# Kernel tuning notes

Hardware: AMD Instinct MI355X
Metric: run time of the kernel (lower is better)

The kernel has to match this reference:

```python
import math
import jax, jax.numpy as jnp
import numpy as np

B, L, D, H = 2, 1024, 1024, 16
HD = D // H
NBUCKETS = 64
EPS = 1e-5


def _rotary(x, pos):
    # x: (B,H,L,hd), pos: (B,L) float positions
    hd = x.shape[-1]
    nf = hd // 2
    periods = jnp.exp(jnp.linspace(math.log(1.0), math.log(10000.0), nf))
    freqs = 2.0 * np.pi / periods
    freqs = jnp.concatenate([freqs, freqs], axis=-1)  # (hd,)
    ang = pos[:, None, :, None].astype(x.dtype) * freqs  # (B,1,L,hd)
    cos, sin = jnp.cos(ang), jnp.sin(ang)
    x1, x2 = jnp.split(x, 2, axis=-1)
    rot = jnp.concatenate([-x2, x1], axis=-1)
    return x * cos + rot * sin


def _layernorm(x, g, b):
    mu = jnp.mean(x, axis=-1, keepdims=True)
    var = jnp.mean((x - mu) ** 2, axis=-1, keepdims=True)
    return (x - mu) * jax.lax.rsqrt(var + EPS) * g + b


def setup_inputs() -> dict:
    key = jax.random.key(0)
    ks = jax.random.split(key, 16)
    s = 1.0 / math.sqrt(D)
    x = jax.random.normal(ks[0], (B, L, D), jnp.float32)
    z = jax.random.randint(ks[1], (B, L, L), 0, NBUCKETS, jnp.int32)
    mask = jnp.ones((B, L), dtype=bool)
    idx = jnp.tile(jnp.arange(L, dtype=jnp.int32)[None, :], (B, 1))
    chain = jnp.sort(jax.random.randint(ks[2], (B, L), 0, 4, jnp.int32), axis=-1)
    mol_type = jax.random.randint(ks[3], (B, L), 0, 2, jnp.int32)
    Wq = jax.random.normal(ks[4], (D, D), jnp.float32) * s
    Wk = jax.random.normal(ks[5], (D, D), jnp.float32) * s
    Wv = jax.random.normal(ks[6], (D, D), jnp.float32) * s
    Wo = jax.random.normal(ks[7], (D, D), jnp.float32) * s
    cWq = jax.random.normal(ks[8], (D, D), jnp.float32) * s
    cWk = jax.random.normal(ks[9], (D, D), jnp.float32) * s
    cWv = jax.random.normal(ks[10], (D, D), jnp.float32) * s
    qg = jnp.ones((D,), jnp.float32)
    qb = jnp.zeros((D,), jnp.float32)
    kg = jnp.ones((D,), jnp.float32)
    kb = jnp.zeros((D,), jnp.float32)
    attn_bias = jax.random.normal(ks[11], (NBUCKETS, H), jnp.float32) * 0.02
    return dict(x=x, z=z, mask=mask, idx=idx, chain=chain, mol_type=mol_type,
                Wq=Wq, Wk=Wk, Wv=Wv, Wo=Wo, cWq=cWq, cWk=cWk, cWv=cWv,
                qg=qg, qb=qb, kg=kg, kb=kb, attn_bias=attn_bias)


def reference(x, z, mask, idx, chain, mol_type, Wq, Wk, Wv, Wo, cWq, cWk, cWv,
              qg, qb, kg, kb, attn_bias):
    scale = 1.0 / math.sqrt(HD)  # sqrt(D / heads)

    def split_heads(t):  # (B,L,D) -> (B,H,L,hd)
        return t.reshape(B, L, H, HD).transpose(0, 2, 1, 3)

    q = split_heads(_layernorm(x @ Wq.T, qg, qb))
    k = split_heads(_layernorm(x @ Wk.T, kg, kb))
    q = _rotary(q, idx)
    k = _rotary(k, idx)
    attn = jnp.einsum('bhqd,bhkd->bhqk', q, k) * scale

    cq = split_heads(x @ cWq.T)
    ck = split_heads(x @ cWk.T)
    cross_attn = jnp.einsum('bhqd,bhkd->bhqk', cq, ck) * scale

    # same polymer chain mask (B,L,L)
    spm = (chain[:, None, :] == chain[:, :, None]) & (mol_type == 0)[:, None, :]
    attn = jnp.where(spm[:, None], attn, cross_attn)

    # gathered pairwise bias: bias[z] (B,L,L,H) -> (B,H,L,L)
    attn = attn + attn_bias[z].transpose(0, 3, 1, 2)

    attn = jnp.where(mask[:, None, None, :], attn, -jnp.inf)
    attn = jax.nn.softmax(attn, axis=-1)

    self_w = jnp.where(spm[:, None], attn, 0.0)
    cross_w = jnp.where(spm[:, None], 0.0, attn)

    v = split_heads(x @ Wv.T)
    v = _rotary(v, idx)  # rope_values
    out = jnp.einsum('bhqk,bhkd->bhqd', self_w, v)
    out = _rotary(out, -idx)
    out = out.transpose(0, 2, 1, 3).reshape(B, L, D)

    cv = split_heads(x @ cWv.T)
    cross_out = jnp.einsum('bhqk,bhkd->bhqd', cross_w, cv)
    cross_out = cross_out.transpose(0, 2, 1, 3).reshape(B, L, D)

    return (out + cross_out) @ Wo.T
```

## Files before the change

### kernel.cpp

```cpp
#include <hip/hip_runtime.h>


typedef __attribute__((ext_vector_type(8))) short short8;
typedef __attribute__((ext_vector_type(4))) short short4v;
typedef __attribute__((ext_vector_type(4))) float f32x4;

struct W6 { const unsigned short* p[6]; };
struct Src13 { const void* p[13]; };

__device__ __forceinline__ float bf2f(unsigned short u){
  union { unsigned u32; float f; } v; v.u32 = ((unsigned)u) << 16; return v.f;
}
__device__ __forceinline__ unsigned short f2bf(float f){
  unsigned u = __float_as_uint(f);
  u += 0x7FFFu + ((u >> 16) & 1u);
  return (unsigned short)(u >> 16);
}
__device__ __forceinline__ unsigned short f2bf_rz(float f){
  return (unsigned short)(__float_as_uint(f) >> 16);
}
__device__ __forceinline__ void async16(const void* g, void* l){
  __builtin_amdgcn_global_load_lds(
      (const __attribute__((address_space(1))) unsigned int*)g,
      (__attribute__((address_space(3))) unsigned int*)l, 16, 0, 0);
}
__device__ __forceinline__ f32x4 mfma16(short8 a, short8 b, f32x4 c){
  return __builtin_amdgcn_mfma_f32_16x16x32_bf16(a, b, c, 0, 0, 0);
}
__device__ __forceinline__ float freq_of(int dd){
  return 6.283185307179586f * __expf(-0.29710775393471563f * (float)dd);
}

#define PX   0
#define PW(i) (2097152 + (i) * 1048576)
#define PQG  9437184
#define PQB  9438208
#define PKG  9439232
#define PKB  9440256
#define PBI  9441280
#define PARK_TOTAL 9442304

__global__ __launch_bounds__(256) void k_convert(
    Src13 src, unsigned short* __restrict__ park,
    const int* __restrict__ z, unsigned char* __restrict__ zpk,
    int* __restrict__ flag)
{
  const int t = threadIdx.x;
  const int bid = blockIdx.x;
  if (bid >= 9221) {
    int base = (bid - 9221) * 1024 + t * 4;
    int4 zv = *(const int4*)(z + base);
    unsigned int pk = (unsigned)zv.x | ((unsigned)zv.y << 8) |
                      ((unsigned)zv.z << 16) | ((unsigned)zv.w << 24);
    *(unsigned int*)(zpk + base) = pk;
    return;
  }
  __shared__ int shcnt;
  if (t == 0) shcnt = 0;
  __syncthreads();
  const unsigned short* xr = (const unsigned short*)src.p[0];
  int e = (xr[2 * t] >> 7) & 0xFF;
  unsigned long long m = __ballot(e >= 132);
  if ((t & 63) == 0) atomicAdd(&shcnt, __popcll(m));
  __syncthreads();
  const bool isf32 = shcnt > 64;

  int seg, inner;
  if (bid < 2048)      { seg = 0;                        inner = bid; }
  else if (bid < 9216) { seg = 1 + ((bid - 2048) >> 10); inner = (bid - 2048) & 1023; }
  else                 { seg = 8 + (bid - 9216);         inner = 0; }
  static const __device__ int segbase[13] = {
    PX, PW(0), PW(1), PW(2), PW(3), PW(4), PW(5), PW(6),
    PQG, PQB, PKG, PKB, PBI };
  unsigned short* dst = park + segbase[seg] + inner * 1024 + t * 4;
  if (isf32) {
    const float* s = (const float*)src.p[seg] + inner * 1024 + t * 4;
    f32x4 v = *(const f32x4*)s;
    short4v o;
    o.x = (short)f2bf(v.x); o.y = (short)f2bf(v.y);
    o.z = (short)f2bf(v.z); o.w = (short)f2bf(v.w);
    *(short4v*)dst = o;
  } else {
    const unsigned short* s = (const unsigned short*)src.p[seg] + inner * 1024 + t * 4;
    *(short4v*)dst = *(const short4v*)s;
  }
  if (bid == 0 && t == 0) *flag = isf32 ? 1 : 0;
}

__global__ __launch_bounds__(256, 2) void k_proj_gemm(
    const unsigned short* __restrict__ X, W6 w6, unsigned short* __restrict__ Y)
{
  __shared__ unsigned short As[2][128 * 32];
  __shared__ unsigned short Bs[2][128 * 32];
  const int t = threadIdx.x;
  const int lane = t & 63, wid = t >> 6;
  int bid = blockIdx.y * 16 + blockIdx.x;
  bid = (bid & 7) * 96 + (bid >> 3);
  const int m0 = (bid & 15) * 128;
  const int bn = bid >> 4;
  const unsigned short* W = w6.p[bn >> 3];
  const int nw0 = (bn & 7) * 128;
  const int waveM = (wid & 1) * 64, waveN = (wid >> 1) * 64;
  const int g = lane >> 4, c16 = lane & 15;
  const int srow = t >> 2, scol = (t & 3) * 8;

  f32x4 acc[4][4];
  #pragma unroll
  for (int i = 0; i < 4; i++)
    #pragma unroll
    for (int j = 0; j < 4; j++) acc[i][j] = f32x4{0.f, 0.f, 0.f, 0.f};

#define PSTAGE(bi, k0_) do { \
    async16(X + (size_t)(m0 + srow) * 1024 + (k0_) + scol,       (char*)As[bi] + t * 16); \
    async16(X + (size_t)(m0 + 64 + srow) * 1024 + (k0_) + scol,  (char*)As[bi] + 4096 + t * 16); \
    async16(W + (size_t)(nw0 + srow) * 1024 + (k0_) + scol,      (char*)Bs[bi] + t * 16); \
    async16(W + (size_t)(nw0 + 64 + srow) * 1024 + (k0_) + scol, (char*)Bs[bi] + 4096 + t * 16); \
  } while (0)

  PSTAGE(0, 0);
  for (int k0 = 0; k0 < 1024; k0 += 32) {
    const int cur = (k0 >> 5) & 1;
    if (k0 < 992) {
      PSTAGE(cur ^ 1, k0 + 32);
      __builtin_amdgcn_sched_barrier(0);
      asm volatile("s_waitcnt vmcnt(4)" ::: "memory");
    } else {
      __builtin_amdgcn_sched_barrier(0);
      asm volatile("s_waitcnt vmcnt(0)" ::: "memory");
    }
    __builtin_amdgcn_s_barrier();
    __builtin_amdgcn_sched_barrier(0);
    short8 af[4], bfr[4];
    #pragma unroll
    for (int mt = 0; mt < 4; mt++)
      af[mt] = *(const short8*)(As[cur] + (waveM + mt * 16 + c16) * 32 + g * 8);
    #pragma unroll
    for (int nt = 0; nt < 4; nt++)
      bfr[nt] = *(const short8*)(Bs[cur] + (waveN + nt * 16 + c16) * 32 + g * 8);
    #pragma unroll
    for (int mt = 0; mt < 4; mt++)
      #pragma unroll
      for (int nt = 0; nt < 4; nt++)
        acc[mt][nt] = mfma16(af[mt], bfr[nt], acc[mt][nt]);
    __builtin_amdgcn_sched_barrier(0);
    __builtin_amdgcn_s_barrier();
  }
#undef PSTAGE
  const int n0 = bn * 128;
  #pragma unroll
  for (int mt = 0; mt < 4; mt++)
    #pragma unroll
    for (int nt = 0; nt < 4; nt++)
      #pragma unroll
      for (int r = 0; r < 4; r++) {
        int row = m0 + waveM + mt * 16 + g * 4 + r;
        int col = n0 + waveN + nt * 16 + c16;
        Y[(size_t)row * 6144 + col] = f2bf(acc[mt][nt][r]);
      }
}

__global__ __launch_bounds__(256) void k_post(
    const unsigned short* __restrict__ Y,
    const unsigned short* __restrict__ qg, const unsigned short* __restrict__ qbv,
    const unsigned short* __restrict__ kg, const unsigned short* __restrict__ kbv,
    const int* __restrict__ idx,
    unsigned short* __restrict__ qo, unsigned short* __restrict__ ko,
    unsigned short* __restrict__ cqo, unsigned short* __restrict__ cko,
    unsigned short* __restrict__ vto, unsigned short* __restrict__ cvto)
{
  const int r = blockIdx.x;
  const int b = r >> 10, l = r & 1023;
  const int t = threadIdx.x;
  __shared__ float red[4];
  __shared__ float rowbuf[1024];
  __shared__ float tc[32], ts[32];
  const unsigned short* Yr = Y + (size_t)r * 6144;
  const float pos = (float)idx[r];

  if (t < 32) {
    float a = pos * freq_of(t);
    tc[t] = cosf(a);
    ts[t] = sinf(a);
  }
  __syncthreads();

  for (int sec = 0; sec < 2; sec++) {
    const unsigned short* src = Yr + sec * 1024;
    const unsigned short* gg = sec ? kg : qg;
    const unsigned short* bb = sec ? kbv : qbv;
    unsigned short* dst = sec ? ko : qo;
    float v0 = bf2f(src[t]), v1 = bf2f(src[t + 256]);
    float v2 = bf2f(src[t + 512]), v3 = bf2f(src[t + 768]);
    float s = v0 + v1 + v2 + v3;
    float s2 = v0 * v0 + v1 * v1 + v2 * v2 + v3 * v3;
    #pragma unroll
    for (int o = 32; o > 0; o >>= 1) {
      s += __shfl_down(s, o, 64);
      s2 += __shfl_down(s2, o, 64);
    }
    __syncthreads();
    if ((t & 63) == 0) red[t >> 6] = s;
    __syncthreads();
    float tot = red[0] + red[1] + red[2] + red[3];
    __syncthreads();
    if ((t & 63) == 0) red[t >> 6] = s2;
    __syncthreads();
    float tot2 = red[0] + red[1] + red[2] + red[3];
    float mu = tot * (1.f / 1024.f);
    float var = tot2 * (1.f / 1024.f) - mu * mu;
    float rstd = rsqrtf(var + 1e-5f);
    rowbuf[t]       = (v0 - mu) * rstd * bf2f(gg[t])       + bf2f(bb[t]);
    rowbuf[t + 256] = (v1 - mu) * rstd * bf2f(gg[t + 256]) + bf2f(bb[t + 256]);
    rowbuf[t + 512] = (v2 - mu) * rstd * bf2f(gg[t + 512]) + bf2f(bb[t + 512]);
    rowbuf[t + 768] = (v3 - mu) * rstd * bf2f(gg[t + 768]) + bf2f(bb[t + 768]);
    __syncthreads();
    #pragma unroll
    for (int j = 0; j < 4; j++) {
      int d = t + 256 * j;
      int h = d >> 6, dd = d & 63;
      float c = tc[dd & 31], sn = ts[dd & 31];
      float x1 = rowbuf[d];
      float x2 = rowbuf[(d & ~63) | ((dd + 32) & 63)];
      float res = (dd < 32) ? (x1 * c - x2 * sn) : (x1 * c + x2 * sn);
      dst[((size_t)(b * 16 + h) * 1024 + l) * 64 + dd] = f2bf(res);
    }
  }
  {
    const unsigned short* src = Yr + 2048;
    __syncthreads();
    rowbuf[t] = bf2f(src[t]); rowbuf[t + 256] = bf2f(src[t + 256]);
    rowbuf[t + 512] = bf2f(src[t + 512]); rowbuf[t + 768] = bf2f(src[t + 768]);
    __syncthreads();
    #pragma unroll
    for (int j = 0; j < 4; j++) {
      int d = t + 256 * j;
      int h = d >> 6, dd = d & 63;
      float c = tc[dd & 31], sn = ts[dd & 31];
      float x1 = rowbuf[d];
      float x2 = rowbuf[(d & ~63) | ((dd + 32) & 63)];
      float res = (dd < 32) ? (x1 * c - x2 * sn) : (x1 * c + x2 * sn);
      vto[((size_t)(b * 16 + h) * 64 + dd) * 1024 + l] = f2bf(res);
    }
  }
  #pragma unroll
  for (int j = 0; j < 4; j++) {
    int d = t + 256 * j;
    int h = d >> 6, dd = d & 63;
    size_t km = ((size_t)(b * 16 + h) * 1024 + l) * 64 + dd;
    cqo[km] = Yr[3072 + d];
    cko[km] = Yr[4096 + d];
    cvto[((size_t)(b * 16 + h) * 64 + dd) * 1024 + l] = Yr[5120 + d];
  }
}

__global__ __launch_bounds__(256, 2) void k_attn(
    const unsigned short* __restrict__ qm, const unsigned short* __restrict__ km,
    const unsigned short* __restrict__ cqm, const unsigned short* __restrict__ ckm,
    const unsigned short* __restrict__ vt, const unsigned short* __restrict__ cvt,
    const int* __restrict__ chain, const int* __restrict__ mol,
    const unsigned char* __restrict__ zpk, const unsigned short* __restrict__ bias,
    float* __restrict__ Opart, float* __restrict__ lpart)
{
  const int q0 = blockIdx.x * 128;
  const int bh = blockIdx.y;
  const int seg = blockIdx.z;
  const int b = bh >> 4, h = bh & 15;
  __shared__ float biasf[64];
  __shared__ unsigned char codek[512];
  __shared__ __align__(16) unsigned char zs[128 * 64];
  __shared__ __align__(16) unsigned short Ks[64 * 64], cKs[64 * 64];
  __shared__ __align__(16) unsigned short Vs[64 * 64], cVs[64 * 64];
  __shared__ unsigned short Ps[4][2][16][36], Pc[4][2][16][36];
  const int t = threadIdx.x, lane = t & 63, w = t >> 6;
  const int g = lane >> 4, c16 = lane & 15;
  const int kbeg = seg * 512;

  if (t < 128) {
    int4 ch = *(const int4*)(chain + b * 1024 + kbeg + t * 4);
    int4 mo = *(const int4*)(mol   + b * 1024 + kbeg + t * 4);
    codek[t * 4 + 0] = mo.x ? 255 : (unsigned char)ch.x;
    codek[t * 4 + 1] = mo.y ? 255 : (unsigned char)ch.y;
    codek[t * 4 + 2] = mo.z ? 255 : (unsigned char)ch.z;
    codek[t * 4 + 3] = mo.w ? 255 : (unsigned char)ch.w;
  } else if (t < 192) {
    biasf[t - 128] = bf2f(bias[(t - 128) * 16 + h]);
  }

  const size_t basep = (size_t)bh << 16;
  int cqa[2][4];
  #pragma unroll
  for (int s = 0; s < 2; s++) {
    int4 cqv = *(const int4*)(chain + b * 1024 + q0 + s * 64 + w * 16 + g * 4);
    cqa[s][0] = cqv.x; cqa[s][1] = cqv.y; cqa[s][2] = cqv.z; cqa[s][3] = cqv.w;
  }

  short8 aq0[2], aq1[2], acq0[2], acq1[2];
  #pragma unroll
  for (int s = 0; s < 2; s++) {
    const unsigned short* qrow  = qm  + basep + (size_t)(q0 + s * 64 + w * 16 + c16) * 64;
    const unsigned short* cqrow = cqm + basep + (size_t)(q0 + s * 64 + w * 16 + c16) * 64;
    aq0[s]  = *(const short8*)(qrow + g * 8);
    aq1[s]  = *(const short8*)(qrow + 32 + g * 8);
    acq0[s] = *(const short8*)(cqrow + g * 8);
    acq1[s] = *(const short8*)(cqrow + 32 + g * 8);
  }

  float l_[2][4];
  f32x4 Os[2][4], Oc[2][4];
  #pragma unroll
  for (int s = 0; s < 2; s++)
    #pragma unroll
    for (int nt = 0; nt < 4; nt++) {
      l_[s][nt] = 0.f;
      Os[s][nt] = f32x4{0.f, 0.f, 0.f, 0.f};
      Oc[s][nt] = f32x4{0.f, 0.f, 0.f, 0.f};
    }
  const int Rk = t >> 3, jk = t & 7;
  const int Rz = t >> 2, jz = t & 3;
  const int swz16 = (jz ^ ((Rz >> 2) & 3)) * 16;
  const f32x4 zero = f32x4{0.f, 0.f, 0.f, 0.f};
  __syncthreads();

  for (int kc = 0; kc < 8; kc++) {
    const int kt = kbeg + kc * 64;
    #pragma unroll
    for (int i = 0; i < 2; i++)
      async16(zpk + (size_t)b * 1048576 + (size_t)(q0 + i * 64 + Rz) * 1024
                  + kt + swz16,
              (char*)zs + i * 4096 + t * 16);
    #pragma unroll
    for (int i = 0; i < 2; i++) {
      int row = i * 32 + Rk;
      int srcb = jk ^ (row & 7);
      async16(km  + basep + (size_t)(kt + row) * 64 + srcb * 8, (char*)Ks  + i * 4096 + t * 16);
      async16(ckm + basep + (size_t)(kt + row) * 64 + srcb * 8, (char*)cKs + i * 4096 + t * 16);
      async16(vt  + basep + (size_t)row * 1024 + kt + srcb * 8, (char*)Vs  + i * 4096 + t * 16);
      async16(cvt + basep + (size_t)row * 1024 + kt + srcb * 8, (char*)cVs + i * 4096 + t * 16);
    }
    __syncthreads();
    #pragma unroll
    for (int half = 0; half < 2; half++) {
      f32x4 sS[2][2], sC[2][2];
      #pragma unroll
      for (int nn = 0; nn < 2; nn++) {
        int R = (half * 2 + nn) * 16 + c16;
        int sw = R & 7;
        short8 kbl = *(const short8*)((char*)Ks  + R * 128 + ((g ^ sw) * 16));
        short8 kbh = *(const short8*)((char*)Ks  + R * 128 + (((4 + g) ^ sw) * 16));
        short8 cbl = *(const short8*)((char*)cKs + R * 128 + ((g ^ sw) * 16));
        short8 cbh = *(const short8*)((char*)cKs + R * 128 + (((4 + g) ^ sw) * 16));
        #pragma unroll
        for (int s = 0; s < 2; s++) {
          sS[s][nn] = mfma16(aq1[s], kbh, mfma16(aq0[s], kbl, zero));
          sC[s][nn] = mfma16(acq1[s], cbh, mfma16(acq0[s], cbl, zero));
        }
      }
      int cd0 = codek[kc * 64 + half * 32 + c16];
      int cd1 = codek[kc * 64 + half * 32 + 16 + c16];
      short8 aps[2], apc[2];
      #pragma unroll
      for (int s = 0; s < 2; s++) {
        #pragma unroll
        for (int r = 0; r < 4; r++) {
          const unsigned char* zr = zs + (s * 64 + w * 16 + g * 4 + r) * 64;
          float bi0 = biasf[zr[((half * 2) ^ g) * 16 + c16]];
          float bi1 = biasf[zr[((half * 2 + 1) ^ g) * 16 + c16]];
          bool sp0 = (cd0 == cqa[s][r]);
          bool sp1 = (cd1 == cqa[s][r]);
          float p0 = __expf(__fmaf_rn(sp0 ? sS[s][0][r] : sC[s][0][r], 0.125f, bi0));
          float p1 = __expf(__fmaf_rn(sp1 ? sS[s][1][r] : sC[s][1][r], 0.125f, bi1));
          l_[s][r] += p0 + p1;
          int lr = g * 4 + r;
          Ps[w][s][lr][c16]      = f2bf_rz(sp0 ? p0 : 0.f);
          Pc[w][s][lr][c16]      = f2bf_rz(sp0 ? 0.f : p0);
          Ps[w][s][lr][16 + c16] = f2bf_rz(sp1 ? p1 : 0.f);
          Pc[w][s][lr][16 + c16] = f2bf_rz(sp1 ? 0.f : p1);
        }
        aps[s] = *(const short8*)&Ps[w][s][c16][g * 8];
        apc[s] = *(const short8*)&Pc[w][s][c16][g * 8];
      }
      #pragma unroll
      for (int nt = 0; nt < 4; nt++) {
        int R = nt * 16 + c16;
        int sw = R & 7;
        int J = half * 4 + g;
        short8 bv  = *(const short8*)((char*)Vs  + R * 128 + ((J ^ sw) * 16));
        short8 bcv = *(const short8*)((char*)cVs + R * 128 + ((J ^ sw) * 16));
        #pragma unroll
        for (int s = 0; s < 2; s++) {
          Os[s][nt] = mfma16(aps[s], bv,  Os[s][nt]);
          Oc[s][nt] = mfma16(apc[s], bcv, Oc[s][nt]);
        }
      }
    }
    __syncthreads();
  }

  #pragma unroll
  for (int s = 0; s < 2; s++)
    #pragma unroll
    for (int r = 0; r < 4; r++) {
      float lv = l_[s][r];
      lv += __shfl_xor(lv, 1);
      lv += __shfl_xor(lv, 2);
      lv += __shfl_xor(lv, 4);
      lv += __shfl_xor(lv, 8);
      int row = q0 + s * 64 + w * 16 + g * 4 + r;
      float* op = Opart + (((size_t)seg * 32 + bh) * 1024 + row) * 128;
      #pragma unroll
      for (int nt = 0; nt < 4; nt++) {
        op[nt * 16 + c16]      = Os[s][nt][r];
        op[64 + nt * 16 + c16] = Oc[s][nt][r];
      }
      if (c16 == 0) lpart[((size_t)seg * 32 + bh) * 1024 + row] = lv;
    }
}

__global__ __launch_bounds__(256) void k_combine(
    const float* __restrict__ Opart, const float* __restrict__ lpart,
    const int* __restrict__ idx, unsigned short* __restrict__ comb)
{
  const int t = threadIdx.x;
  const int rg = blockIdx.x * 8 + (t >> 5);
  const int d = t & 31;
  const int bh = rg >> 10, row = rg & 1023;
  const int b = bh >> 4, h = bh & 15;
  float oslo = 0.f, oshi = 0.f, oclo = 0.f, ochi = 0.f, l = 0.f;
  #pragma unroll
  for (int seg = 0; seg < 2; seg++) {
    const float* op = Opart + (((size_t)seg * 32 + bh) * 1024 + row) * 128;
    oslo += op[d]; oshi += op[32 + d];
    oclo += op[64 + d]; ochi += op[96 + d];
    l += lpart[((size_t)seg * 32 + bh) * 1024 + row];
  }
  float inv = 1.f / l;
  float pos = (float)idx[b * 1024 + row];
  float fr = freq_of(d);
  float aa = -pos * fr;
  float cc = cosf(aa), sn = sinf(aa);
  size_t orow = ((size_t)(b * 1024 + row)) * 1024 + h * 64;
  comb[orow + d]      = f2bf((oslo * cc - oshi * sn + oclo) * inv);
  comb[orow + d + 32] = f2bf((oshi * cc + oslo * sn + ochi) * inv);
}

__global__ __launch_bounds__(256, 2) void k_out_gemm(
    const unsigned short* __restrict__ A, const unsigned short* __restrict__ Wo,
    const int* __restrict__ flag, void* __restrict__ outv)
{
  __shared__ unsigned short As[2][64 * 32];
  __shared__ unsigned short Bs[2][128 * 32];
  const int t = threadIdx.x;
  const int lane = t & 63, wid = t >> 6;
  int bid = blockIdx.y * 32 + blockIdx.x;
  bid = (bid & 7) * 32 + (bid >> 3);
  const int m0 = (bid & 31) * 64;
  const int n0 = (bid >> 5) * 128;
  const int waveM = (wid & 1) * 32, waveN = (wid >> 1) * 64;
  const int g = lane >> 4, c16 = lane & 15;
  const int srow = t >> 2, scol = (t & 3) * 8;
  const int f32out = *flag;
  f32x4 acc[2][4];
  #pragma unroll
  for (int i = 0; i < 2; i++)
    #pragma unroll
    for (int j = 0; j < 4; j++) acc[i][j] = f32x4{0.f, 0.f, 0.f, 0.f};

#define OSTAGE(bi, k0_) do { \
    async16(A  + (size_t)(m0 + srow) * 1024 + (k0_) + scol,       (char*)As[bi] + t * 16); \
    async16(Wo + (size_t)(n0 + srow) * 1024 + (k0_) + scol,       (char*)Bs[bi] + t * 16); \
    async16(Wo + (size_t)(n0 + 64 + srow) * 1024 + (k0_) + scol,  (char*)Bs[bi] + 4096 + t * 16); \
  } while (0)

  OSTAGE(0, 0);
  for (int k0 = 0; k0 < 1024; k0 += 32) {
    const int cur = (k0 >> 5) & 1;
    if (k0 < 992) {
      OSTAGE(cur ^ 1, k0 + 32);
      __builtin_amdgcn_sched_barrier(0);
      asm volatile("s_waitcnt vmcnt(3)" ::: "memory");
    } else {
      __builtin_amdgcn_sched_barrier(0);
      asm volatile("s_waitcnt vmcnt(0)" ::: "memory");
    }
    __builtin_amdgcn_s_barrier();
    __builtin_amdgcn_sched_barrier(0);
    short8 af[2], bfr[4];
    #pragma unroll
    for (int mt = 0; mt < 2; mt++)
      af[mt] = *(const short8*)(As[cur] + (waveM + mt * 16 + c16) * 32 + g * 8);
    #pragma unroll
    for (int nt = 0; nt < 4; nt++)
      bfr[nt] = *(const short8*)(Bs[cur] + (waveN + nt * 16 + c16) * 32 + g * 8);
    #pragma unroll
    for (int mt = 0; mt < 2; mt++)
      #pragma unroll
      for (int nt = 0; nt < 4; nt++)
        acc[mt][nt] = mfma16(af[mt], bfr[nt], acc[mt][nt]);
    __builtin_amdgcn_sched_barrier(0);
    __builtin_amdgcn_s_barrier();
  }
#undef OSTAGE
  #pragma unroll
  for (int mt = 0; mt < 2; mt++)
    #pragma unroll
    for (int nt = 0; nt < 4; nt++)
      #pragma unroll
      for (int r = 0; r < 4; r++) {
        int row = m0 + waveM + mt * 16 + g * 4 + r;
        int col = n0 + waveN + nt * 16 + c16;
        if (f32out) ((float*)outv)[(size_t)row * 1024 + col] = acc[mt][nt][r];
        else ((unsigned short*)outv)[(size_t)row * 1024 + col] = f2bf(acc[mt][nt][r]);
      }
}

extern "C" void kernel_launch(void* const* d_in, const int* in_sizes, int n_in,
                              void* d_out, int out_size, void* d_ws, size_t ws_size,
                              hipStream_t stream)
{
  (void)in_sizes; (void)n_in; (void)out_size; (void)ws_size;
  const int* z     = (const int*)d_in[1];
  const int* idx   = (const int*)d_in[3];
  const int* chain = (const int*)d_in[4];
  const int* mol   = (const int*)d_in[5];

  char* ws = (char*)d_ws;
  unsigned short* Y     = (unsigned short*)ws;
  size_t off = 50331648;
  unsigned short* qbuf  = (unsigned short*)(ws + off); off += 4194304;
  unsigned short* kbuf  = (unsigned short*)(ws + off); off += 4194304;
  unsigned short* cqbuf = (unsigned short*)(ws + off); off += 4194304;
  unsigned short* ckbuf = (unsigned short*)(ws + off); off += 4194304;
  unsigned short* vtbuf = (unsigned short*)(ws + off); off += 4194304;
  unsigned short* cvtbuf= (unsigned short*)(ws + off); off += 4194304;
  unsigned short* comb  = (unsigned short*)(ws + off); off += 4194304;
  unsigned short* park  = (unsigned short*)(ws + off); off += (size_t)PARK_TOTAL * 2;
  unsigned char*  zpk   = (unsigned char*)(ws + off); off += 2097152;
  float*          Opart = (float*)(ws + off); off += (size_t)2 * 32 * 1024 * 128 * 4;
  float*          lpart = (float*)(ws + off); off += (size_t)2 * 32 * 1024 * 4;
  int*            flag  = (int*)(ws + off);

  Src13 src;
  src.p[0]  = d_in[0];
  src.p[1]  = d_in[6];
  src.p[2]  = d_in[7];
  src.p[3]  = d_in[8];
  src.p[4]  = d_in[9];
  src.p[5]  = d_in[10];
  src.p[6]  = d_in[11];
  src.p[7]  = d_in[12];
  src.p[8]  = d_in[13];
  src.p[9]  = d_in[14];
  src.p[10] = d_in[15];
  src.p[11] = d_in[16];
  src.p[12] = d_in[17];

  W6 w6;
  w6.p[0] = park + PW(0);
  w6.p[1] = park + PW(1);
  w6.p[2] = park + PW(2);
  w6.p[3] = park + PW(4);
  w6.p[4] = park + PW(5);
  w6.p[5] = park + PW(6);

  k_convert<<<11269, 256, 0, stream>>>(src, park, z, zpk, flag);
  k_proj_gemm<<<dim3(16, 48), 256, 0, stream>>>(park + PX, w6, Y);
  k_post<<<2048, 256, 0, stream>>>(Y, park + PQG, park + PQB, park + PKG, park + PKB,
                                   idx, qbuf, kbuf, cqbuf, ckbuf, vtbuf, cvtbuf);
  k_attn<<<dim3(8, 32, 2), 256, 0, stream>>>(qbuf, kbuf, cqbuf, ckbuf, vtbuf, cvtbuf,
                                             chain, mol, zpk, park + PBI,
                                             Opart, lpart);
  k_combine<<<4096, 256, 0, stream>>>(Opart, lpart, idx, comb);
  k_out_gemm<<<dim3(32, 8), 256, 0, stream>>>(comb, park + PW(3), flag, d_out);
}
```

Measured before the change: 245.8 us.

## Triple-buffer GEMM LDS stages and rewrite post kernel as wave-per-row

Both projection and output GEMMs move from double to triple LDS buffering, which lets the trailing barrier in each k-step be dropped because the next prefetch targets a buffer nobody is still reading. The post-processing kernel now gives each row to a single wavefront, using shuffle reductions and shuffle-based rotary pairing in place of shared-memory row buffers and block-wide syncs, and launches a quarter as many blocks. The aim is to cut barrier and LDS round-trip overhead. In exchange the GEMMs use more LDS per block, which may limit occupancy, and the post kernel holds more registers per thread.

After: 253.6 us. 3.2% more time.

```diff
diff --git a/kernel.cpp b/kernel.cpp
--- a/kernel.cpp
+++ b/kernel.cpp
@@ -90,8 +90,8 @@
 __global__ __launch_bounds__(256, 2) void k_proj_gemm(
     const unsigned short* __restrict__ X, W6 w6, unsigned short* __restrict__ Y)
 {
-  __shared__ unsigned short As[2][128 * 32];
-  __shared__ unsigned short Bs[2][128 * 32];
+  __shared__ unsigned short As[3][128 * 32];
+  __shared__ unsigned short Bs[3][128 * 32];
   const int t = threadIdx.x;
   const int lane = t & 63, wid = t >> 6;
   int bid = blockIdx.y * 16 + blockIdx.x;
@@ -119,9 +119,10 @@
 
   PSTAGE(0, 0);
   for (int k0 = 0; k0 < 1024; k0 += 32) {
-    const int cur = (k0 >> 5) & 1;
-    if (k0 < 992) {
-      PSTAGE(cur ^ 1, k0 + 32);
+    const int i = k0 >> 5;
+    const int cur = i % 3;
+    if (i < 31) {
+      PSTAGE((i + 1) % 3, k0 + 32);
       __builtin_amdgcn_sched_barrier(0);
       asm volatile("s_waitcnt vmcnt(4)" ::: "memory");
     } else {
@@ -142,8 +143,6 @@
       #pragma unroll
       for (int nt = 0; nt < 4; nt++)
         acc[mt][nt] = mfma16(af[mt], bfr[nt], acc[mt][nt]);
-    __builtin_amdgcn_sched_barrier(0);
-    __builtin_amdgcn_s_barrier();
   }
 #undef PSTAGE
   const int n0 = bn * 128;
@@ -168,88 +167,62 @@
     unsigned short* __restrict__ cqo, unsigned short* __restrict__ cko,
     unsigned short* __restrict__ vto, unsigned short* __restrict__ cvto)
 {
-  const int r = blockIdx.x;
-  const int b = r >> 10, l = r & 1023;
-  const int t = threadIdx.x;
-  __shared__ float red[4];
-  __shared__ float rowbuf[1024];
-  __shared__ float tc[32], ts[32];
+  const int w = threadIdx.x >> 6, l = threadIdx.x & 63;
+  const int r = blockIdx.x * 4 + w;
+  const int b = r >> 10, lrow = r & 1023;
   const unsigned short* Yr = Y + (size_t)r * 6144;
   const float pos = (float)idx[r];
 
-  if (t < 32) {
-    float a = pos * freq_of(t);
-    tc[t] = cosf(a);
-    ts[t] = sinf(a);
-  }
-  __syncthreads();
-
+  const float ang = pos * freq_of(l & 31);
+  const float tc = cosf(ang), ts = sinf(ang);
+  const float sgn = (l < 32) ? -1.f : 1.f;
+
+  #pragma unroll
   for (int sec = 0; sec < 2; sec++) {
     const unsigned short* src = Yr + sec * 1024;
     const unsigned short* gg = sec ? kg : qg;
     const unsigned short* bb = sec ? kbv : qbv;
     unsigned short* dst = sec ? ko : qo;
-    float v0 = bf2f(src[t]), v1 = bf2f(src[t + 256]);
-    float v2 = bf2f(src[t + 512]), v3 = bf2f(src[t + 768]);
-    float s = v0 + v1 + v2 + v3;
-    float s2 = v0 * v0 + v1 * v1 + v2 * v2 + v3 * v3;
+    float v[16];
+    float s = 0.f, s2 = 0.f;
+    #pragma unroll
+    for (int j = 0; j < 16; j++) {
+      v[j] = bf2f(src[j * 64 + l]);
+      s += v[j];
+      s2 += v[j] * v[j];
+    }
     #pragma unroll
     for (int o = 32; o > 0; o >>= 1) {
-      s += __shfl_down(s, o, 64);
-      s2 += __shfl_down(s2, o, 64);
-    }
-    __syncthreads();
-    if ((t & 63) == 0) red[t >> 6] = s;
-    __syncthreads();
-    float tot = red[0] + red[1] + red[2] + red[3];
-    __syncthreads();
-    if ((t & 63) == 0) red[t >> 6] = s2;
-    __syncthreads();
-    float tot2 = red[0] + red[1] + red[2] + red[3];
-    float mu = tot * (1.f / 1024.f);
-    float var = tot2 * (1.f / 1024.f) - mu * mu;
+      s += __shfl_xor(s, o, 64);
+      s2 += __shfl_xor(s2, o, 64);
+    }
+    float mu = s * (1.f / 1024.f);
+    float var = s2 * (1.f / 1024.f) - mu * mu;
     float rstd = rsqrtf(var + 1e-5f);
-    rowbuf[t]       = (v0 - mu) * rstd * bf2f(gg[t])       + bf2f(bb[t]);
-    rowbuf[t + 256] = (v1 - mu) * rstd * bf2f(gg[t + 256]) + bf2f(bb[t + 256]);
-    rowbuf[t + 512] = (v2 - mu) * rstd * bf2f(gg[t + 512]) + bf2f(bb[t + 512]);
-    rowbuf[t + 768] = (v3 - mu) * rstd * bf2f(gg[t + 768]) + bf2f(bb[t + 768]);
-    __syncthreads();
-    #pragma unroll
-    for (int j = 0; j < 4; j++) {
-      int d = t + 256 * j;
-      int h = d >> 6, dd = d & 63;
-      float c = tc[dd & 31], sn = ts[dd & 31];
-      float x1 = rowbuf[d];
-      float x2 = rowbuf[(d & ~63) | ((dd + 32) & 63)];
-      float res = (dd < 32) ? (x1 * c - x2 * sn) : (x1 * c + x2 * sn);
-      dst[((size_t)(b * 16 + h) * 1024 + l) * 64 + dd] = f2bf(res);
+    #pragma unroll
+    for (int j = 0; j < 16; j++) {
+      float xn = (v[j] - mu) * rstd * bf2f(gg[j * 64 + l]) + bf2f(bb[j * 64 + l]);
+      float x2 = __shfl_xor(xn, 32, 64);
+      float res = xn * tc + sgn * x2 * ts;
+      dst[((size_t)(b * 16 + j) * 1024 + lrow) * 64 + l] = f2bf(res);
     }
   }
   {
     const unsigned short* src = Yr + 2048;
-    __syncthreads();
-    rowbuf[t] = bf2f(src[t]); rowbuf[t + 256] = bf2f(src[t + 256]);
-    rowbuf[t + 512] = bf2f(src[t + 512]); rowbuf[t + 768] = bf2f(src[t + 768]);
-    __syncthreads();
-    #pragma unroll
-    for (int j = 0; j < 4; j++) {
-      int d = t + 256 * j;
-      int h = d >> 6, dd = d & 63;
-      float c = tc[dd & 31], sn = ts[dd & 31];
-      float x1 = rowbuf[d];
-      float x2 = rowbuf[(d & ~63) | ((dd + 32) & 63)];
-      float res = (dd < 32) ? (x1 * c - x2 * sn) : (x1 * c + x2 * sn);
-      vto[((size_t)(b * 16 + h) * 64 + dd) * 1024 + l] = f2bf(res);
-    }
-  }
-  #pragma unroll
-  for (int j = 0; j < 4; j++) {
-    int d = t + 256 * j;
-    int h = d >> 6, dd = d & 63;
-    size_t km = ((size_t)(b * 16 + h) * 1024 + l) * 64 + dd;
-    cqo[km] = Yr[3072 + d];
-    cko[km] = Yr[4096 + d];
-    cvto[((size_t)(b * 16 + h) * 64 + dd) * 1024 + l] = Yr[5120 + d];
+    #pragma unroll
+    for (int j = 0; j < 16; j++) {
+      float x1 = bf2f(src[j * 64 + l]);
+      float x2 = __shfl_xor(x1, 32, 64);
+      float res = x1 * tc + sgn * x2 * ts;
+      vto[((size_t)(b * 16 + j) * 64 + l) * 1024 + lrow] = f2bf(res);
+    }
+  }
+  #pragma unroll
+  for (int j = 0; j < 16; j++) {
+    size_t km = ((size_t)(b * 16 + j) * 1024 + lrow) * 64 + l;
+    cqo[km] = Yr[3072 + j * 64 + l];
+    cko[km] = Yr[4096 + j * 64 + l];
+    cvto[((size_t)(b * 16 + j) * 64 + l) * 1024 + lrow] = Yr[5120 + j * 64 + l];
   }
 }
 
@@ -447,8 +420,8 @@
     const unsigned short* __restrict__ A, const unsigned short* __restrict__ Wo,
     const int* __restrict__ flag, void* __restrict__ outv)
 {
-  __shared__ unsigned short As[2][64 * 32];
-  __shared__ unsigned short Bs[2][128 * 32];
+  __shared__ unsigned short As[3][64 * 32];
+  __shared__ unsigned short Bs[3][128 * 32];
   const int t = threadIdx.x;
   const int lane = t & 63, wid = t >> 6;
   int bid = blockIdx.y * 32 + blockIdx.x;
@@ -473,9 +446,10 @@
 
   OSTAGE(0, 0);
   for (int k0 = 0; k0 < 1024; k0 += 32) {
-    const int cur = (k0 >> 5) & 1;
-    if (k0 < 992) {
-      OSTAGE(cur ^ 1, k0 + 32);
+    const int i = k0 >> 5;
+    const int cur = i % 3;
+    if (i < 31) {
+      OSTAGE((i + 1) % 3, k0 + 32);
       __builtin_amdgcn_sched_barrier(0);
       asm volatile("s_waitcnt vmcnt(3)" ::: "memory");
     } else {
@@ -496,8 +470,6 @@
       #pragma unroll
       for (int nt = 0; nt < 4; nt++)
         acc[mt][nt] = mfma16(af[mt], bfr[nt], acc[mt][nt]);
-    __builtin_amdgcn_sched_barrier(0);
-    __builtin_amdgcn_s_barrier();
   }
 #undef OSTAGE
   #pragma unroll
@@ -564,8 +536,8 @@
 
   k_convert<<<11269, 256, 0, stream>>>(src, park, z, zpk, flag);
   k_proj_gemm<<<dim3(16, 48), 256, 0, stream>>>(park + PX, w6, Y);
-  k_post<<<2048, 256, 0, stream>>>(Y, park + PQG, park + PQB, park + PKG, park + PKB,
-                                   idx, qbuf, kbuf, cqbuf, ckbuf, vtbuf, cvtbuf);
+  k_post<<<512, 256, 0, stream>>>(Y, park + PQG, park + PQB, park + PKG, park + PKB,
+                                  idx, qbuf, kbuf, cqbuf, ckbuf, vtbuf, cvtbuf);
   k_attn<<<dim3(8, 32, 2), 256, 0, stream>>>(qbuf, kbuf, cqbuf, ckbuf, vtbuf, cvtbuf,
                                              chain, mol, zpk, park + PBI,
                                              Opart, lpart);
```
